# Kernel optimization log

Hardware: AMD Instinct MI355X
Metric: run time of the kernel (lower is better)

The kernel has to match this reference:

```python
import jax, jax.numpy as jnp
import numpy as np

NPOINT = 2048  # S after transition-down (init npoint)
NSAMPLE = 16   # K neighbors (init nsample)
EPS = 1e-5     # BatchNorm eps


def _conv1d(w, b, x):  # w [O,I], x [B,I,N] -> [B,O,N]
    y = jnp.einsum('oi,bin->bon', w, x)
    return y if b is None else y + b[None, :, None]


def _conv2d(w, b, x):  # w [O,I], x [B,I,S,K] -> [B,O,S,K]
    y = jnp.einsum('oi,bisk->bosk', w, x)
    return y if b is None else y + b[None, :, None, None]


def _gather(x, idx):  # x [B,C,N], idx [B,S] -> [B,C,S]
    return jax.vmap(lambda xb, ib: xb[:, ib])(x, idx)


def _group(x, idx):  # x [B,C,N], idx [B,S,K] -> [B,C,S,K]
    return jax.vmap(lambda xb, ib: xb[:, ib])(x, idx)


def _fps(xyz_bnc, S):  # farthest point sampling, start at index 0 (deterministic)
    B, N, _ = xyz_bnc.shape
    def body(carry, _):
        dist, far = carry
        centroid = jnp.take_along_axis(xyz_bnc, far[:, None, None], axis=1)  # [B,1,3]
        d = jnp.sum((xyz_bnc - centroid) ** 2, axis=-1)  # [B,N]
        dist = jnp.minimum(dist, d)
        nxt = jnp.argmax(dist, axis=-1).astype(jnp.int32)
        return (dist, nxt), far
    init = (jnp.full((B, N), 1e10, xyz_bnc.dtype), jnp.zeros((B,), jnp.int32))
    _, idxs = jax.lax.scan(body, init, None, length=S)
    return jnp.transpose(idxs)  # [B,S]


def _knn(k, query, pts):  # query [B,S,3], pts [B,N,3] -> idx [B,S,k]
    d2 = (jnp.sum(query ** 2, -1)[..., None] + jnp.sum(pts ** 2, -1)[:, None, :]
          - 2.0 * jnp.einsum('bsc,bnc->bsn', query, pts))
    _, idx = jax.lax.top_k(-d2, k)
    return idx


def _bn(x, gamma, beta):  # training-mode batchnorm over (B, spatial) per channel
    axes = (0,) + tuple(range(2, x.ndim))
    m = jnp.mean(x, axes, keepdims=True)
    v = jnp.var(x, axes, keepdims=True)
    shp = (1, -1) + (1,) * (x.ndim - 2)
    return gamma.reshape(shp) * (x - m) / jnp.sqrt(v + EPS) + beta.reshape(shp)


def _forward(xyz, points, td_w, td_b, td_gamma, td_beta,
             blk_before_w, blk_before_b, blk_qkv_w,
             blk_pos_w1, blk_pos_b1, blk_pos_w2, blk_pos_b2,
             blk_attn_w1, blk_attn_b1, blk_attn_w2, blk_attn_b2,
             blk_after_w, blk_after_b):
    S, K = NPOINT, NSAMPLE
    xyz_t = jnp.transpose(xyz, (0, 2, 1))  # [B,N,3]
    # ---- PointTransformerTransitionDown ----
    fps_idx = _fps(xyz_t, S)                       # [B,S]
    new_xyz = _gather(xyz, fps_idx)                # [B,3,S]
    new_xyz_t = jnp.transpose(new_xyz, (0, 2, 1))  # [B,S,3]
    gidx = _knn(K, new_xyz_t, xyz_t)               # [B,S,K]
    grouped_xyz = _group(xyz, gidx) - new_xyz[:, :, :, None]   # [B,3,S,K]
    grouped = jnp.concatenate([_group(points, gidx), grouped_xyz], axis=1)  # [B,D+3,S,K]
    h = jax.nn.relu(_bn(_conv2d(td_w, td_b, grouped), td_gamma, td_beta))
    pts = jnp.max(h, axis=-1)  # [B,out,S]
    # ---- PointTransformerResBlocks ----
    sgidx = _knn(K, new_xyz_t, new_xyz_t)          # self-KNN [B,S,K]
    gxyz = new_xyz[:, :, :, None] - _group(new_xyz, sgidx)  # [B,3,S,K]
    num_attn = blk_before_w.shape[0]
    for i in range(num_attn):
        rel = _conv2d(blk_pos_w2[i], blk_pos_b2[i],
                      jax.nn.relu(_conv2d(blk_pos_w1[i], blk_pos_b1[i], gxyz)))  # [B,mid,S,K]
        p = _conv1d(blk_before_w[i], blk_before_b[i], pts)   # [B,mid,S]
        qkv = _conv1d(blk_qkv_w[i], None, p)                 # [B,3*mid,S]
        q, k_, v = jnp.split(qkv, 3, axis=1)
        qk_rel = q[:, :, :, None] - _group(k_, sgidx)        # [B,mid,S,K]
        v = _group(v, sgidx) + rel
        sim = _conv2d(blk_attn_w2[i], blk_attn_b2[i],
                      jax.nn.relu(_conv2d(blk_attn_w1[i], blk_attn_b1[i], qk_rel + rel)))
        attn = jax.nn.softmax(sim, axis=-1)                  # softmax over neighbors
        agg = jnp.sum(attn * v, axis=-1)                     # [B,mid,S]
        pts = pts + _conv1d(blk_after_w[i], blk_after_b[i], agg)
    return new_xyz, pts


def setup_inputs() -> dict:
    key = jax.random.key(0)
    ks = jax.random.split(key, 20)
    B, N, Din, Dout, mid, A = 4, 8192, 64, 128, 32, 2
    r = lambda k, s, sc: sc * jax.random.normal(k, s, dtype=jnp.float32)
    return {
        'xyz': r(ks[0], (B, 3, N), 1.0),
        'points': r(ks[1], (B, Din, N), 1.0),
        'td_w': r(ks[2], (Dout, Din + 3), 0.1), 'td_b': r(ks[3], (Dout,), 0.02),
        'td_gamma': jnp.ones((Dout,), jnp.float32), 'td_beta': jnp.zeros((Dout,), jnp.float32),
        'blk_before_w': r(ks[4], (A, mid, Dout), 0.1), 'blk_before_b': r(ks[5], (A, mid), 0.02),
        'blk_qkv_w': r(ks[6], (A, 3 * mid, mid), 0.1),
        'blk_pos_w1': r(ks[7], (A, 64, 3), 0.1), 'blk_pos_b1': r(ks[8], (A, 64), 0.02),
        'blk_pos_w2': r(ks[9], (A, mid, 64), 0.1), 'blk_pos_b2': r(ks[10], (A, mid), 0.02),
        'blk_attn_w1': r(ks[11], (A, 4 * mid, mid), 0.1), 'blk_attn_b1': r(ks[12], (A, 4 * mid), 0.02),
        'blk_attn_w2': r(ks[13], (A, mid, 4 * mid), 0.1), 'blk_attn_b2': r(ks[14], (A, mid), 0.02),
        'blk_after_w': r(ks[15], (A, Dout, mid), 0.1), 'blk_after_b': r(ks[16], (A, Dout), 0.02),
    }


def reference(xyz, points, td_w, td_b, td_gamma, td_beta,
              blk_before_w, blk_before_b, blk_qkv_w,
              blk_pos_w1, blk_pos_b1, blk_pos_w2, blk_pos_b2,
              blk_attn_w1, blk_attn_b1, blk_attn_w2, blk_attn_b2,
              blk_after_w, blk_after_b):
    return _forward(xyz, points, td_w, td_b, td_gamma, td_beta,
                    blk_before_w, blk_before_b, blk_qkv_w,
                    blk_pos_w1, blk_pos_b1, blk_pos_w2, blk_pos_b2,
                    blk_attn_w1, blk_attn_b1, blk_attn_w2, blk_attn_b2,
                    blk_after_w, blk_after_b)
```

## Files before the change

### kernel.cpp

```cpp
#include <hip/hip_runtime.h>

#define BB 4
#define NN 8192
#define SS 2048
#define KK 16

typedef float v2f __attribute__((ext_vector_type(2)));

#define FTH 512
#define FPT (NN/FTH)
__global__ __launch_bounds__(FTH, 1) void fps_kernel(
    const float* __restrict__ xyz,
    float* __restrict__ out_newxyz,
    float* __restrict__ nxt)
{
  #pragma clang fp contract(off)
  const int b = blockIdx.x;
  const int tid = threadIdx.x;
  const int wave = tid >> 6;
  const int lane = tid & 63;
  const float* xb = xyz + b*3*NN;
  __shared__ float sx[NN], sy[NN], sz[NN];
  __shared__ __align__(16) float smax[8];
  __shared__ unsigned gidx_slot[2];
  __shared__ int smi[SS];
  v2f px[FPT/2], py[FPT/2], pz[FPT/2], dist[FPT/2];
  #pragma unroll
  for (int j = 0; j < FPT; ++j) {
    int i = tid + j*FTH;
    float x = xb[i], y = xb[NN+i], z = xb[2*NN+i];
    asm volatile("" : "+v"(x), "+v"(y), "+v"(z));
    ((float*)px)[j] = x; ((float*)py)[j] = y; ((float*)pz)[j] = z;
    ((float*)dist)[j] = 1e10f;
  }
  #pragma unroll
  for (int j = 0; j < FPT; ++j) {
    int i = tid + j*FTH;
    sx[i] = ((float*)px)[j]; sy[i] = ((float*)py)[j]; sz[i] = ((float*)pz)[j];
  }
  if (tid == 0) { smi[0] = 0; gidx_slot[0] = 0xFFFFFFFFu; gidx_slot[1] = 0xFFFFFFFFu; }
  float cx = xb[0], cy = xb[NN], cz = xb[2*NN];
  __syncthreads();
  for (int it = 1; it < SS; ++it) {
    const int buf = it & 1;
    v2f cx2 = {cx, cx}, cy2 = {cy, cy}, cz2 = {cz, cz};
    v2f vmax = {-1.0f, -1.0f};
    #pragma unroll
    for (int j = 0; j < FPT/2; ++j) {
      v2f dx = px[j] - cx2, dy = py[j] - cy2, dz = pz[j] - cz2;
      v2f d = dx*dx + dy*dy;
      d = d + dz*dz;
      v2f nd = __builtin_elementwise_min(dist[j], d);
      dist[j] = nd;
      vmax = __builtin_elementwise_max(vmax, nd);
    }
    float mloc = fmaxf(vmax.x, vmax.y);
    float m = mloc;
    #define FPS_DPP(ctrl) { \
      float s = __int_as_float(__builtin_amdgcn_update_dpp(0, __float_as_int(m), ctrl, 0xf, 0xf, true)); \
      m = fmaxf(m, s); }
    FPS_DPP(0x111)
    FPS_DPP(0x112)
    FPS_DPP(0x114)
    FPS_DPP(0x118)
    FPS_DPP(0x142)
    FPS_DPP(0x143)
    #undef FPS_DPP
    if (lane == 63) smax[wave] = m;
    __syncthreads();
    if (tid == 0) gidx_slot[1 - buf] = 0xFFFFFFFFu;
    float4 s0 = ((const float4*)smax)[0];
    float4 s1 = ((const float4*)smax)[1];
    float M = fmaxf(fmaxf(fmaxf(s0.x, s0.y), fmaxf(s0.z, s0.w)),
                    fmaxf(fmaxf(s1.x, s1.y), fmaxf(s1.z, s1.w)));
    if (mloc == M) {
      int idx = 0x7FFFFFFF;
      #pragma unroll
      for (int j = FPT/2 - 1; j >= 0; --j) {
        if (dist[j].y == M) idx = tid + (2*j+1)*FTH;
        if (dist[j].x == M) idx = tid + (2*j)*FTH;
      }
      atomicMin(&gidx_slot[buf], (unsigned)idx);
    }
    __syncthreads();
    int mi = (int)gidx_slot[buf];
    if (tid == 0) smi[it] = mi;
    cx = sx[mi]; cy = sy[mi]; cz = sz[mi];
  }
  __syncthreads();
  for (int it = tid; it < SS; it += FTH) {
    int mi = smi[it];
    float x = sx[mi], y = sy[mi], z = sz[mi];
    out_newxyz[(b*3+0)*SS + it] = x;
    out_newxyz[(b*3+1)*SS + it] = y;
    out_newxyz[(b*3+2)*SS + it] = z;
    nxt[(b*SS+it)*3+0] = x; nxt[(b*SS+it)*3+1] = y; nxt[(b*SS+it)*3+2] = z;
  }
}

#define TILE 2048
#define KTH 256
__global__ __launch_bounds__(KTH) void knn_kernel(
    const float* __restrict__ query_t,
    const float* __restrict__ cand1,
    const float* __restrict__ cand2,
    int* __restrict__ out1,
    int* __restrict__ out2)
{
  #pragma clang fp contract(off)
  __shared__ float4 sc[TILE];
  __shared__ float  smd[4*64*17];
  __shared__ int    smj[4*64*17];
  const int blocksPerB = SS/64;
  const int half = blockIdx.x >> 7;
  const int blk = blockIdx.x & 127;
  const float* cand = half ? cand2 : cand1;
  const int Nc = half ? SS : NN;
  int* outidx = half ? out2 : out1;
  const int b = blk / blocksPerB;
  const int q0 = (blk % blocksPerB)*64;
  const int wave = threadIdx.x >> 6, lane = threadIdx.x & 63;
  const int s = q0 + lane;
  const float qx = query_t[(b*SS+s)*3+0];
  const float qy = query_t[(b*SS+s)*3+1];
  const float qz = query_t[(b*SS+s)*3+2];
  float sq = qx*qx + qy*qy; sq = sq + qz*qz;
  float d16[16]; int i16[16];
  #pragma unroll
  for (int j = 0; j < 16; ++j) { d16[j] = 1e30f; i16[j] = 0x7FFFFFFF; }
  const float* cb = cand + b*3*Nc;
  const int QL = TILE/4;
  for (int base = 0; base < Nc; base += TILE) {
    __syncthreads();
    for (int j = threadIdx.x; j < TILE; j += KTH) {
      float x = cb[base+j], y = cb[Nc+base+j], z = cb[2*Nc+base+j];
      float pp = x*x + y*y; pp = pp + z*z;
      sc[j] = make_float4(x, y, z, pp);
    }
    __syncthreads();
    const int lo = wave*QL, hi = lo + QL;
    for (int j = lo; j < hi; ++j) {
      float4 c = sc[j];
      float qp = qx*c.x + qy*c.y; qp = qp + qz*c.z;
      float d2 = (sq + c.w) - 2.0f*qp;
      if (d2 < d16[15]) {
        d16[15] = d2; i16[15] = base + j;
        #pragma unroll
        for (int t = 15; t > 0; --t) {
          if (d16[t] < d16[t-1]) {
            float td = d16[t]; d16[t] = d16[t-1]; d16[t-1] = td;
            int   ti = i16[t]; i16[t] = i16[t-1]; i16[t-1] = ti;
          }
        }
      }
    }
  }
  const int off = (wave*64 + lane)*17;
  #pragma unroll
  for (int j = 0; j < 16; ++j) { smd[off+j] = d16[j]; smj[off+j] = i16[j]; }
  __syncthreads();
  if (wave == 0) {
    int p[4] = {0,0,0,0};
    for (int o = 0; o < 16; ++o) {
      float bd = 3e38f; int bi = 0x7FFFFFFF, bw = 0;
      #pragma unroll
      for (int w = 0; w < 4; ++w) {
        float d = smd[(w*64+lane)*17 + p[w]];
        int   i = smj[(w*64+lane)*17 + p[w]];
        if (d < bd || (d == bd && i < bi)) { bd = d; bi = i; bw = w; }
      }
      p[bw]++;
      outidx[(b*SS+s)*KK + o] = bi;
    }
  }
}

__global__ __launch_bounds__(128) void td_kernel(
    const float* __restrict__ points,
    const float* __restrict__ xyz,
    const float* __restrict__ newxyz,
    const int* __restrict__ gidx,
    const float* __restrict__ td_w,
    const float* __restrict__ td_b,
    float* __restrict__ ymax,
    float* __restrict__ psum,
    float* __restrict__ psq)
{
  const int bs = blockIdx.x;
  const int b = bs >> 11, s = bs & (SS-1);
  const int t = threadIdx.x;
  __shared__ int gi[KK];
  __shared__ float g[67][KK];
  if (t < KK) gi[t] = gidx[bs*KK + t];
  __syncthreads();
  for (int idx = t; idx < 67*KK; idx += 128) {
    int i = idx >> 4, k = idx & 15;
    float v;
    if (i < 64) v = points[(b*64+i)*NN + gi[k]];
    else {
      int c = i - 64;
      v = xyz[(b*3+c)*NN + gi[k]] - newxyz[(b*3+c)*SS + s];
    }
    g[i][k] = v;
  }
  __syncthreads();
  float acc[KK];
  #pragma unroll
  for (int k = 0; k < KK; ++k) acc[k] = 0.0f;
  const float* wrow = td_w + t*67;
  for (int i = 0; i < 67; ++i) {
    float w = wrow[i];
    #pragma unroll
    for (int k = 0; k < KK; ++k) acc[k] = fmaf(w, g[i][k], acc[k]);
  }
  float bias = td_b[t];
  float mx = -1e30f, s1 = 0.f, s2 = 0.f;
  #pragma unroll
  for (int k = 0; k < KK; ++k) {
    float y = acc[k] + bias;
    mx = fmaxf(mx, y);
    s1 += y;
    s2 = fmaf(y, y, s2);
  }
  ymax[bs*128 + t] = mx;
  psum[bs*128 + t] = s1;
  psq [bs*128 + t] = s2;
}

__global__ __launch_bounds__(256) void bn_partial(
    const float* __restrict__ psum, const float* __restrict__ psq,
    float* __restrict__ part1, float* __restrict__ part2)
{
  const int blk = blockIdx.x, t = threadIdx.x;
  const int c = t & 127, half = t >> 7;
  const float* ps = psum + (blk*64 + half*32)*128;
  const float* pq = psq  + (blk*64 + half*32)*128;
  float s1 = 0.f, s2 = 0.f;
  for (int r = 0; r < 32; ++r) { s1 += ps[r*128 + c]; s2 += pq[r*128 + c]; }
  __shared__ float sh1[256], sh2[256];
  sh1[t] = s1; sh2[t] = s2;
  __syncthreads();
  if (t < 128) {
    part1[blk*128 + t] = sh1[t] + sh1[t+128];
    part2[blk*128 + t] = sh2[t] + sh2[t+128];
  }
}

__global__ __launch_bounds__(128) void bn_final(
    const float* __restrict__ part1, const float* __restrict__ part2,
    const float* __restrict__ gamma, const float* __restrict__ beta,
    float* __restrict__ scale, float* __restrict__ bias)
{
  const int o = threadIdx.x;
  float s1 = 0.f, s2 = 0.f;
  for (int j = 0; j < 128; ++j) { s1 += part1[j*128+o]; s2 += part2[j*128+o]; }
  const float n = (float)(BB*SS*KK);
  float mean = s1/n;
  float var  = s2/n - mean*mean;
  float sc = gamma[o] / sqrtf(var + 1e-5f);
  scale[o] = sc;
  bias[o]  = beta[o] - mean*sc;
}

__global__ __launch_bounds__(128) void r1_first(
    const float* __restrict__ ymax,
    const float* __restrict__ scale, const float* __restrict__ bias,
    const float* __restrict__ bw, const float* __restrict__ bb,
    const float* __restrict__ qw,
    float* __restrict__ pts,
    float* __restrict__ qkv)
{
  const int bs = blockIdx.x;
  const int t = threadIdx.x;
  __shared__ float pcol[128];
  __shared__ float p[32];
  float v = fmaxf(fmaf(ymax[bs*128 + t], scale[t], bias[t]), 0.0f);
  pts[bs*128 + t] = v;
  pcol[t] = v;
  __syncthreads();
  if (t < 32) {
    float acc = 0.f;
    const float* w = bw + t*128;
    for (int j = 0; j < 128; ++j) acc = fmaf(w[j], pcol[j], acc);
    p[t] = acc + bb[t];
  }
  __syncthreads();
  if (t < 96) {
    float acc = 0.f;
    const float* w = qw + t*32;
    #pragma unroll
    for (int j = 0; j < 32; ++j) acc = fmaf(w[j], p[j], acc);
    qkv[bs*96 + t] = acc;
  }
}

__global__ __launch_bounds__(128) void r1_kernel(
    const float* __restrict__ pts,
    const float* __restrict__ bw, const float* __restrict__ bb,
    const float* __restrict__ qw,
    float* __restrict__ qkv)
{
  const int bs = blockIdx.x;
  const int t = threadIdx.x;
  __shared__ float pcol[128];
  __shared__ float p[32];
  pcol[t] = pts[bs*128 + t];
  __syncthreads();
  if (t < 32) {
    float acc = 0.f;
    const float* w = bw + t*128;
    for (int j = 0; j < 128; ++j) acc = fmaf(w[j], pcol[j], acc);
    p[t] = acc + bb[t];
  }
  __syncthreads();
  if (t < 96) {
    float acc = 0.f;
    const float* w = qw + t*32;
    #pragma unroll
    for (int j = 0; j < 32; ++j) acc = fmaf(w[j], p[j], acc);
    qkv[bs*96 + t] = acc;
  }
}

__global__ __launch_bounds__(128) void r2_kernel(
    const float* __restrict__ qkv,
    const float* __restrict__ newxyz,
    const int* __restrict__ sgidx,
    const float* __restrict__ pw1, const float* __restrict__ pb1,
    const float* __restrict__ pw2, const float* __restrict__ pb2,
    const float* __restrict__ aw1, const float* __restrict__ ab1,
    const float* __restrict__ aw2, const float* __restrict__ ab2,
    const float* __restrict__ fw,  const float* __restrict__ fb,
    float* __restrict__ pts)
{
  const int bs = blockIdx.x;
  const int b = bs >> 11, s = bs & (SS-1);
  const int t = threadIdx.x;
  __shared__ int sgi[KK];
  __shared__ float qv[32];
  __shared__ float kn[32*17], vn[32*17];
  __shared__ float gx[3*KK];
  __shared__ float h1[64*KK];
  __shared__ float x2[32*KK];
  __shared__ float a1[128*17];
  __shared__ float simb[32*KK];
  __shared__ float agg[32];
  if (t < KK) sgi[t] = sgidx[bs*KK + t];
  __syncthreads();
  if (t < 32) qv[t] = qkv[bs*96 + t];
  for (int idx = t; idx < 32*KK; idx += 128) {
    int k = idx >> 5, c = idx & 31;
    int base = (b*SS + sgi[k])*96;
    kn[c*17+k] = qkv[base + 32 + c];
    vn[c*17+k] = qkv[base + 64 + c];
  }
  if (t < 3*KK) {
    int c = t >> 4, k = t & 15;
    gx[t] = newxyz[(b*3+c)*SS + s] - newxyz[(b*3+c)*SS + sgi[k]];
  }
  __syncthreads();
  for (int idx = t; idx < 64*KK; idx += 128) {
    int c = idx >> 4, k = idx & 15;
    float acc = 0.f;
    #pragma unroll
    for (int j = 0; j < 3; ++j) acc = fmaf(pw1[c*3+j], gx[j*KK+k], acc);
    h1[idx] = fmaxf(acc + pb1[c], 0.0f);
  }
  __syncthreads();
  for (int idx = t; idx < 32*KK; idx += 128) {
    int c = idx >> 4, k = idx & 15;
    float acc = 0.f;
    const float* w = pw2 + c*64;
    for (int j = 0; j < 64; ++j) acc = fmaf(w[j], h1[j*KK+k], acc);
    float r = acc + pb2[c];
    x2[idx] = (qv[c] - kn[c*17+k]) + r;
    vn[c*17+k] = vn[c*17+k] + r;
  }
  __syncthreads();
  {
    float acc[KK];
    #pragma unroll
    for (int k = 0; k < KK; ++k) acc[k] = 0.f;
    const float* w = aw1 + t*32;
    for (int j = 0; j < 32; ++j) {
      float wv = w[j];
      #pragma unroll
      for (int k = 0; k < KK; ++k) acc[k] = fmaf(wv, x2[j*KK+k], acc[k]);
    }
    float bv = ab1[t];
    #pragma unroll
    for (int k = 0; k < KK; ++k) a1[t*17+k] = fmaxf(acc[k] + bv, 0.0f);
  }
  __syncthreads();
  for (int idx = t; idx < 32*KK; idx += 128) {
    int c = idx >> 4, k = idx & 15;
    float acc = 0.f;
    const float* w = aw2 + c*128;
    for (int j = 0; j < 128; ++j) acc = fmaf(w[j], a1[j*17+k], acc);
    simb[idx] = acc + ab2[c];
  }
  __syncthreads();
  if (t < 32) {
    float m = -1e30f;
    #pragma unroll
    for (int k = 0; k < KK; ++k) m = fmaxf(m, simb[t*KK+k]);
    float sum = 0.f;
    float e[KK];
    #pragma unroll
    for (int k = 0; k < KK; ++k) { e[k] = __expf(simb[t*KK+k] - m); sum += e[k]; }
    float inv = 1.0f / sum;
    float a = 0.f;
    #pragma unroll
    for (int k = 0; k < KK; ++k) a = fmaf(e[k]*inv, vn[t*17+k], a);
    agg[t] = a;
  }
  __syncthreads();
  {
    float acc = 0.f;
    const float* w = fw + t*32;
    #pragma unroll
    for (int j = 0; j < 32; ++j) acc = fmaf(w[j], agg[j], acc);
    pts[bs*128 + t] += acc + fb[t];
  }
}

__global__ __launch_bounds__(256) void transpose_out(
    const float* __restrict__ pts, float* __restrict__ out)
{
  __shared__ float tile[32][33];
  const int b = blockIdx.z;
  const int s0 = blockIdx.x*32, c0 = blockIdx.y*32;
  const int x = threadIdx.x, y = threadIdx.y;
  #pragma unroll
  for (int i = y; i < 32; i += 8)
    tile[i][x] = pts[(b*SS + s0+i)*128 + c0+x];
  __syncthreads();
  #pragma unroll
  for (int i = y; i < 32; i += 8)
    out[(b*128 + c0+i)*SS + s0 + x] = tile[x][i];
}

extern "C" void kernel_launch(void* const* d_in, const int* in_sizes, int n_in,
                              void* d_out, int out_size, void* d_ws, size_t ws_size,
                              hipStream_t stream) {
  const float* xyz      = (const float*)d_in[0];
  const float* points   = (const float*)d_in[1];
  const float* td_w     = (const float*)d_in[2];
  const float* td_b     = (const float*)d_in[3];
  const float* td_gamma = (const float*)d_in[4];
  const float* td_beta  = (const float*)d_in[5];
  const float* bw  = (const float*)d_in[6];
  const float* bb  = (const float*)d_in[7];
  const float* qw  = (const float*)d_in[8];
  const float* pw1 = (const float*)d_in[9];
  const float* pb1 = (const float*)d_in[10];
  const float* pw2 = (const float*)d_in[11];
  const float* pb2 = (const float*)d_in[12];
  const float* aw1 = (const float*)d_in[13];
  const float* ab1 = (const float*)d_in[14];
  const float* aw2 = (const float*)d_in[15];
  const float* ab2 = (const float*)d_in[16];
  const float* fw  = (const float*)d_in[17];
  const float* fb  = (const float*)d_in[18];
  float* out = (float*)d_out;
  float* out_newxyz = out;
  float* out_pts    = out + BB*3*SS;

  char* w = (char*)d_ws;
  float* nxt    = (float*)w; w += BB*SS*3*sizeof(float);
  int*   gidx   = (int*)w;   w += BB*SS*KK*sizeof(int);
  int*   sgidx  = (int*)w;   w += BB*SS*KK*sizeof(int);
  float* ymax   = (float*)w; w += BB*128*SS*sizeof(float);
  float* psum   = (float*)w; w += 128*BB*SS*sizeof(float);
  float* psq    = (float*)w; w += 128*BB*SS*sizeof(float);
  float* part1  = (float*)w; w += 128*128*sizeof(float);
  float* part2  = (float*)w; w += 128*128*sizeof(float);
  float* bnscale= (float*)w; w += 256*sizeof(float);
  float* bnbias = (float*)w; w += 256*sizeof(float);
  float* pts    = (float*)w; w += BB*128*SS*sizeof(float);
  float* qkv    = (float*)w; w += BB*96*SS*sizeof(float);

  fps_kernel<<<BB, FTH, 0, stream>>>(xyz, out_newxyz, nxt);
  knn_kernel<<<2*BB*(SS/64), KTH, 0, stream>>>(nxt, xyz, out_newxyz, gidx, sgidx);
  td_kernel<<<BB*SS, 128, 0, stream>>>(points, xyz, out_newxyz, gidx, td_w, td_b, ymax, psum, psq);
  bn_partial<<<128, 256, 0, stream>>>(psum, psq, part1, part2);
  bn_final<<<1, 128, 0, stream>>>(part1, part2, td_gamma, td_beta, bnscale, bnbias);
  r1_first<<<BB*SS, 128, 0, stream>>>(ymax, bnscale, bnbias, bw, bb, qw, pts, qkv);
  r2_kernel<<<BB*SS, 128, 0, stream>>>(qkv, out_newxyz, sgidx,
      pw1, pb1, pw2, pb2, aw1, ab1, aw2, ab2, fw, fb, pts);
  r1_kernel<<<BB*SS, 128, 0, stream>>>(pts, bw + 32*128, bb + 32, qw + 96*32, qkv);
  r2_kernel<<<BB*SS, 128, 0, stream>>>(qkv, out_newxyz, sgidx,
      pw1 + 64*3, pb1 + 64, pw2 + 32*64, pb2 + 32,
      aw1 + 128*32, ab1 + 128, aw2 + 32*128, ab2 + 32,
      fw + 128*32, fb + 128, pts);
  dim3 tg(SS/32, 128/32, BB), tb(32, 8);
  transpose_out<<<tg, tb, 0, stream>>>(pts, out_pts);
}
```

Measured before the change: 2.774 ms.

## Cut FPS per-iteration barriers from two to one using per-wave max/index slots

Each wave now computes its own max and its lowest index at that max, writing both to per-wave slots in a triple-buffered shared array. After a single barrier every thread reduces the 8 (max, index) pairs with a lexicographic compare. This replaces the old two-barrier scheme (global max, then atomicMin on a global index). It removes one block-wide barrier per FPS iteration at the cost of a small serial 8-way reduction done by every thread. Comparing the float max as unsigned bits is valid because distances are non-negative.

Measured after the change: 3.775 ms. 1.36x slower.

```diff
diff --git a/kernel.cpp b/kernel.cpp
--- a/kernel.cpp
+++ b/kernel.cpp
@@ -21,8 +21,8 @@
   const int lane = tid & 63;
   const float* xb = xyz + b*3*NN;
   __shared__ float sx[NN], sy[NN], sz[NN];
-  __shared__ __align__(16) float smax[8];
-  __shared__ unsigned gidx_slot[2];
+  __shared__ __align__(16) unsigned slotHi[3][8];
+  __shared__ __align__(16) unsigned slotLo[3][8];
   __shared__ int smi[SS];
   v2f px[FPT/2], py[FPT/2], pz[FPT/2], dist[FPT/2];
   #pragma unroll
@@ -38,11 +38,13 @@
     int i = tid + j*FTH;
     sx[i] = ((float*)px)[j]; sy[i] = ((float*)py)[j]; sz[i] = ((float*)pz)[j];
   }
-  if (tid == 0) { smi[0] = 0; gidx_slot[0] = 0xFFFFFFFFu; gidx_slot[1] = 0xFFFFFFFFu; }
+  if (tid == 0) smi[0] = 0;
+  if (tid < 24) ((unsigned*)slotLo)[tid] = 0xFFFFFFFFu;
   float cx = xb[0], cy = xb[NN], cz = xb[2*NN];
   __syncthreads();
   for (int it = 1; it < SS; ++it) {
-    const int buf = it & 1;
+    const int buf = it % 3;
+    const int nxtbuf = (it + 1) % 3;
     v2f cx2 = {cx, cx}, cy2 = {cy, cy}, cz2 = {cz, cz};
     v2f vmax = {-1.0f, -1.0f};
     #pragma unroll
@@ -66,24 +68,26 @@
     FPS_DPP(0x142)
     FPS_DPP(0x143)
     #undef FPS_DPP
-    if (lane == 63) smax[wave] = m;
-    __syncthreads();
-    if (tid == 0) gidx_slot[1 - buf] = 0xFFFFFFFFu;
-    float4 s0 = ((const float4*)smax)[0];
-    float4 s1 = ((const float4*)smax)[1];
-    float M = fmaxf(fmaxf(fmaxf(s0.x, s0.y), fmaxf(s0.z, s0.w)),
-                    fmaxf(fmaxf(s1.x, s1.y), fmaxf(s1.z, s1.w)));
-    if (mloc == M) {
+    float wm = __int_as_float(__builtin_amdgcn_readlane(__float_as_int(m), 63));
+    if (lane == 63) slotHi[buf][wave] = __float_as_uint(wm);
+    if (mloc == wm) {
       int idx = 0x7FFFFFFF;
       #pragma unroll
       for (int j = FPT/2 - 1; j >= 0; --j) {
-        if (dist[j].y == M) idx = tid + (2*j+1)*FTH;
-        if (dist[j].x == M) idx = tid + (2*j)*FTH;
+        if (dist[j].y == wm) idx = tid + (2*j+1)*FTH;
+        if (dist[j].x == wm) idx = tid + (2*j)*FTH;
       }
-      atomicMin(&gidx_slot[buf], (unsigned)idx);
-    }
+      atomicMin(&slotLo[buf][wave], (unsigned)idx);
+    }
+    if (tid < 8) slotLo[nxtbuf][tid] = 0xFFFFFFFFu;
     __syncthreads();
-    int mi = (int)gidx_slot[buf];
+    unsigned bh = slotHi[buf][0], bl = slotLo[buf][0];
+    #pragma unroll
+    for (int w = 1; w < 8; ++w) {
+      unsigned h = slotHi[buf][w], l = slotLo[buf][w];
+      if (h > bh || (h == bh && l < bl)) { bh = h; bl = l; }
+    }
+    int mi = (int)bl;
     if (tid == 0) smi[it] = mi;
     cx = sx[mi]; cy = sy[mi]; cz = sz[mi];
   }
```

## Transpose point features for coalesced gather and widen KNN blocks to 8 waves

Applied to the files above, without the earlier changes.

Adds a kernel that transposes the point features to a point-major [B,N,64] layout, so the grouping gather in the transition-down kernel reads 64 contiguous channels per neighbour instead of strided scattered loads. It also raises the KNN block from 4 to 8 waves, so each wave scans half as many candidates, and the final merge walks 8 sorted lists. The cost is an extra transpose pass, a workspace buffer, and a longer serial merge in wave 0.

Result: faster. 2.677 ms (-3.5%).

```diff
diff --git a/kernel.cpp b/kernel.cpp
--- a/kernel.cpp
+++ b/kernel.cpp
@@ -98,8 +98,24 @@
   }
 }
 
+__global__ __launch_bounds__(256) void transpose_pts(
+    const float* __restrict__ p, float* __restrict__ o)
+{
+  __shared__ float tile[32][33];
+  const int b = blockIdx.z;
+  const int n0 = blockIdx.x*32, c0 = blockIdx.y*32;
+  const int x = threadIdx.x, y = threadIdx.y;
+  #pragma unroll
+  for (int i = y; i < 32; i += 8)
+    tile[i][x] = p[(b*64 + c0+i)*NN + n0+x];
+  __syncthreads();
+  #pragma unroll
+  for (int i = y; i < 32; i += 8)
+    o[(b*NN + n0+i)*64 + c0+x] = tile[x][i];
+}
+
 #define TILE 2048
-#define KTH 256
+#define KTH 512
 __global__ __launch_bounds__(KTH) void knn_kernel(
     const float* __restrict__ query_t,
     const float* __restrict__ cand1,
@@ -109,8 +125,8 @@
 {
   #pragma clang fp contract(off)
   __shared__ float4 sc[TILE];
-  __shared__ float  smd[4*64*17];
-  __shared__ int    smj[4*64*17];
+  __shared__ float  smd[8*64*17];
+  __shared__ int    smj[8*64*17];
   const int blocksPerB = SS/64;
   const int half = blockIdx.x >> 7;
   const int blk = blockIdx.x & 127;
@@ -129,7 +145,7 @@
   #pragma unroll
   for (int j = 0; j < 16; ++j) { d16[j] = 1e30f; i16[j] = 0x7FFFFFFF; }
   const float* cb = cand + b*3*Nc;
-  const int QL = TILE/4;
+  const int QL = TILE/8;
   for (int base = 0; base < Nc; base += TILE) {
     __syncthreads();
     for (int j = threadIdx.x; j < TILE; j += KTH) {
@@ -160,11 +176,11 @@
   for (int j = 0; j < 16; ++j) { smd[off+j] = d16[j]; smj[off+j] = i16[j]; }
   __syncthreads();
   if (wave == 0) {
-    int p[4] = {0,0,0,0};
+    int p[8] = {0,0,0,0,0,0,0,0};
     for (int o = 0; o < 16; ++o) {
       float bd = 3e38f; int bi = 0x7FFFFFFF, bw = 0;
       #pragma unroll
-      for (int w = 0; w < 4; ++w) {
+      for (int w = 0; w < 8; ++w) {
         float d = smd[(w*64+lane)*17 + p[w]];
         int   i = smj[(w*64+lane)*17 + p[w]];
         if (d < bd || (d == bd && i < bi)) { bd = d; bi = i; bw = w; }
@@ -176,7 +192,7 @@
 }
 
 __global__ __launch_bounds__(128) void td_kernel(
-    const float* __restrict__ points,
+    const float* __restrict__ ptst,
     const float* __restrict__ xyz,
     const float* __restrict__ newxyz,
     const int* __restrict__ gidx,
@@ -190,18 +206,18 @@
   const int b = bs >> 11, s = bs & (SS-1);
   const int t = threadIdx.x;
   __shared__ int gi[KK];
-  __shared__ float g[67][KK];
+  __shared__ float g[67*17];
   if (t < KK) gi[t] = gidx[bs*KK + t];
   __syncthreads();
-  for (int idx = t; idx < 67*KK; idx += 128) {
-    int i = idx >> 4, k = idx & 15;
-    float v;
-    if (i < 64) v = points[(b*64+i)*NN + gi[k]];
-    else {
-      int c = i - 64;
-      v = xyz[(b*3+c)*NN + gi[k]] - newxyz[(b*3+c)*SS + s];
-    }
-    g[i][k] = v;
+  #pragma unroll
+  for (int base = 0; base < 1024; base += 128) {
+    int idx = base + t;
+    int i = idx & 63, k = idx >> 6;
+    g[i*17 + k] = ptst[(b*NN + gi[k])*64 + i];
+  }
+  if (t < 48) {
+    int c = t >> 4, k = t & 15;
+    g[(64+c)*17 + k] = xyz[(b*3+c)*NN + gi[k]] - newxyz[(b*3+c)*SS + s];
   }
   __syncthreads();
   float acc[KK];
@@ -211,7 +227,7 @@
   for (int i = 0; i < 67; ++i) {
     float w = wrow[i];
     #pragma unroll
-    for (int k = 0; k < KK; ++k) acc[k] = fmaf(w, g[i][k], acc[k]);
+    for (int k = 0; k < KK; ++k) acc[k] = fmaf(w, g[i*17 + k], acc[k]);
   }
   float bias = td_b[t];
   float mx = -1e30f, s1 = 0.f, s2 = 0.f;
@@ -479,10 +495,15 @@
   float* bnbias = (float*)w; w += 256*sizeof(float);
   float* pts    = (float*)w; w += BB*128*SS*sizeof(float);
   float* qkv    = (float*)w; w += BB*96*SS*sizeof(float);
+  float* ptst   = (float*)w; w += BB*NN*64*sizeof(float);
 
   fps_kernel<<<BB, FTH, 0, stream>>>(xyz, out_newxyz, nxt);
+  {
+    dim3 tg(NN/32, 2, BB), tb(32, 8);
+    transpose_pts<<<tg, tb, 0, stream>>>(points, ptst);
+  }
   knn_kernel<<<2*BB*(SS/64), KTH, 0, stream>>>(nxt, xyz, out_newxyz, gidx, sgidx);
-  td_kernel<<<BB*SS, 128, 0, stream>>>(points, xyz, out_newxyz, gidx, td_w, td_b, ymax, psum, psq);
+  td_kernel<<<BB*SS, 128, 0, stream>>>(ptst, xyz, out_newxyz, gidx, td_w, td_b, ymax, psum, psq);
   bn_partial<<<128, 256, 0, stream>>>(psum, psq, part1, part2);
   bn_final<<<1, 128, 0, stream>>>(part1, part2, td_gamma, td_beta, bnscale, bnbias);
   r1_first<<<BB*SS, 128, 0, stream>>>(ymax, bnscale, bnbias, bw, bb, qw, pts, qkv);
```
